# Performance work log

Hardware: AMD Instinct MI355X
Metric: run time of the kernel (lower is better)

The kernel has to match this reference:

```python
import jax, jax.numpy as jnp
import numpy as np

N_HEAD = 16
N_FEAT = 1024
D_HEAD = N_FEAT // N_HEAD


def setup_inputs() -> dict:
    key = jax.random.key(0)
    ks = jax.random.split(key, 12)
    B, L, T = 8, 128, 64
    s = 0.05
    return {
        "q": jax.random.normal(ks[0], (B, 1, N_FEAT), jnp.float32),
        "kv": jax.random.normal(ks[1], (B, L, T, N_FEAT), jnp.float32),
        "Wq": jax.random.normal(ks[2], (D_HEAD, D_HEAD), jnp.float32) * s,
        "bq": jax.random.normal(ks[3], (D_HEAD,), jnp.float32) * s,
        "Wk": jax.random.normal(ks[4], (D_HEAD, D_HEAD), jnp.float32) * s,
        "bk": jax.random.normal(ks[5], (D_HEAD,), jnp.float32) * s,
        "Wv": jax.random.normal(ks[6], (D_HEAD, D_HEAD), jnp.float32) * s,
        "bv": jax.random.normal(ks[7], (D_HEAD,), jnp.float32) * s,
        "Wo": jax.random.normal(ks[8], (N_FEAT, N_FEAT), jnp.float32) * s,
        "bo": jax.random.normal(ks[9], (N_FEAT,), jnp.float32) * s,
    }


def reference(q, kv, Wq, bq, Wk, bk, Wv, bv, Wo, bo):
    B, L, T, D = kv.shape
    H, dh = N_HEAD, D_HEAD
    # mean-pool q over its singleton length dim and kv over T for keys
    qm = q.mean(axis=-2)                      # [B, D]
    km = kv.mean(axis=-2)                     # [B, L, D]
    qh = qm.reshape(B, H, dh)                 # [B, H, dh]
    kh = km.reshape(B, L, H, dh)              # [B, L, H, dh]
    vh = kv.reshape(B, L, T, H, dh)           # [B, L, T, H, dh]
    # per-head linear projections (torch Linear: x @ W.T + b)
    qh = qh @ Wq.T + bq
    kh = kh @ Wk.T + bk
    vh = vh @ Wv.T + bv
    # faithful transpose chain from the original module
    qh = jnp.swapaxes(qh, -2, -3)             # [H, B, dh]  (3D: swaps B and H)
    kh = jnp.swapaxes(kh, -2, -3)             # [B, H, L, dh]
    # broadcasted matmul -> cross-batch attention [B, H, B, L]
    attw = jnp.matmul(qh, jnp.swapaxes(kh, -1, -2)) / jnp.sqrt(jnp.float32(dh))
    attn = jax.nn.softmax(attw, axis=-1)      # [B, H, B, L]
    # value reshuffle: [B,L,T,H,dh] -> [B,H,T,L,dh] -> [B,H,T,dh,L] -> [B,H,T*dh,L]
    v = jnp.swapaxes(vh, -2, -4)
    v = jnp.swapaxes(v, -1, -2)
    v = v.reshape(B, H, T * dh, L)
    ct = jnp.matmul(attn, jnp.swapaxes(v, -1, -2))   # [B, H, B, T*dh]
    ct = ct.reshape(B, H, B, T, dh)
    ct = jnp.swapaxes(ct, -2, -4)                    # [B, T, B, H, dh]
    ct = ct.reshape(B, T, B, H * dh)                 # [B, T, B, D]
    return ct @ Wo.T + bo
```

## Files before the change

### kernel.cpp

```cpp
#include <hip/hip_runtime.h>
#include <hip/hip_bf16.h>

#define BDIM 8
#define LDIM 128
#define TDIM 64
#define NFEAT 1024
#define HNUM 16
#define DH 64

#define GM 4096
#define GN 1024
#define GK 1024

typedef __attribute__((ext_vector_type(8))) short short8;
typedef __attribute__((ext_vector_type(4))) float f32x4;

__device__ __forceinline__ unsigned short f2bf(float x) {
  union { float f; unsigned u; } v; v.f = x;
  unsigned r = v.u + 0x7fffu + ((v.u >> 16) & 1u);
  return (unsigned short)(r >> 16);
}

__device__ __forceinline__ void gload_lds16(const void* g, void* l) {
  __builtin_amdgcn_global_load_lds((const __attribute__((address_space(1))) void*)g,
                                   (__attribute__((address_space(3))) void*)l, 16, 0, 0);
}

__global__ __launch_bounds__(256) void mean_weff_kernel(
    const float* __restrict__ kv, const float* __restrict__ Wo,
    const float* __restrict__ Wv, const float* __restrict__ bv,
    const float* __restrict__ bo, float* __restrict__ km,
    unsigned short* __restrict__ Weff, float* __restrict__ beff) {
  __shared__ float worow[NFEAT];
  __shared__ float red[256];
  const int bl = blockIdx.x;
  const int tid = threadIdx.x;
  {
    const float* src = kv + (size_t)bl * (TDIM * NFEAT) + tid * 4;
    float4 acc = make_float4(0.f, 0.f, 0.f, 0.f);
    for (int t0 = 0; t0 < TDIM; t0 += 8) {
      float4 v[8];
#pragma unroll
      for (int jj = 0; jj < 8; ++jj)
        v[jj] = *(const float4*)(src + (t0 + jj) * NFEAT);
#pragma unroll
      for (int jj = 0; jj < 8; ++jj) {
        acc.x += v[jj].x; acc.y += v[jj].y; acc.z += v[jj].z; acc.w += v[jj].w;
      }
    }
    const float s = 1.f / TDIM;
    const float4 o = make_float4(acc.x * s, acc.y * s, acc.z * s, acc.w * s);
    *(float4*)(km + (size_t)bl * NFEAT + tid * 4) = o;
  }
  {
    const int f = bl;
    *(float4*)(worow + tid * 4) = *(const float4*)(Wo + (size_t)f * NFEAT + tid * 4);
    __syncthreads();
    const int g0 = tid * 4;
    const int hbase = (g0 >> 6) << 6;
    const int i0 = g0 & 63;
    float a0 = 0, a1 = 0, a2 = 0, a3 = 0;
#pragma unroll 4
    for (int d = 0; d < DH; ++d) {
      const float wod = worow[hbase + d];
      const float4 wv4 = *(const float4*)(Wv + d * DH + i0);
      a0 += wod * wv4.x; a1 += wod * wv4.y; a2 += wod * wv4.z; a3 += wod * wv4.w;
    }
    ushort4 pk;
    pk.x = f2bf(a0); pk.y = f2bf(a1); pk.z = f2bf(a2); pk.w = f2bf(a3);
    *(ushort4*)(Weff + (size_t)f * NFEAT + g0) = pk;
    red[tid] = worow[g0 + 0] * bv[i0 + 0] + worow[g0 + 1] * bv[i0 + 1] +
               worow[g0 + 2] * bv[i0 + 2] + worow[g0 + 3] * bv[i0 + 3];
    __syncthreads();
    for (int sft = 128; sft > 0; sft >>= 1) {
      if (tid < sft) red[tid] += red[tid + sft];
      __syncthreads();
    }
    if (tid == 0) beff[f] = bo[f] + red[0];
  }
}

__global__ __launch_bounds__(128) void attn_kernel(const float* __restrict__ q,
                                                   const float* __restrict__ km,
                                                   const float* __restrict__ Wq,
                                                   const float* __restrict__ bq,
                                                   const float* __restrict__ Wk,
                                                   float* __restrict__ attn) {
  __shared__ float qp_s[BDIM * DH];
  __shared__ float qk_s[BDIM * DH];
  __shared__ float sw[BDIM * LDIM];
  __shared__ float mred[BDIM], ired[BDIM];
  const int b1 = blockIdx.x;
  const int h  = blockIdx.y;
  const int tid = threadIdx.x;

  {
    const int e0 = tid * 4;
    const int b2 = e0 >> 6;
    const int d0 = e0 & 63;
    float a0 = bq[d0], a1 = bq[d0 + 1], a2 = bq[d0 + 2], a3 = bq[d0 + 3];
    const float* qrow = q + b2 * NFEAT + h * DH;
#pragma unroll 4
    for (int i = 0; i < DH; ++i) {
      const float qv = qrow[i];
      a0 += qv * Wq[(d0 + 0) * DH + i];
      a1 += qv * Wq[(d0 + 1) * DH + i];
      a2 += qv * Wq[(d0 + 2) * DH + i];
      a3 += qv * Wq[(d0 + 3) * DH + i];
    }
    qp_s[e0 + 0] = a0; qp_s[e0 + 1] = a1; qp_s[e0 + 2] = a2; qp_s[e0 + 3] = a3;
  }
  __syncthreads();
  {
    const int e0 = tid * 4;
    const int b2 = e0 >> 6;
    const int i0 = e0 & 63;
    float a0 = 0, a1 = 0, a2 = 0, a3 = 0;
#pragma unroll 4
    for (int d = 0; d < DH; ++d) {
      const float qpv = qp_s[b2 * DH + d];
      const float4 wk4 = *(const float4*)(Wk + d * DH + i0);
      a0 += qpv * wk4.x; a1 += qpv * wk4.y; a2 += qpv * wk4.z; a3 += qpv * wk4.w;
    }
    qk_s[e0 + 0] = a0; qk_s[e0 + 1] = a1; qk_s[e0 + 2] = a2; qk_s[e0 + 3] = a3;
  }
  __syncthreads();
  {
    const float* kmrow = km + (size_t)(b1 * LDIM + tid) * NFEAT + h * DH;
    float s[8] = {0, 0, 0, 0, 0, 0, 0, 0};
#pragma unroll
    for (int i4 = 0; i4 < DH / 4; ++i4) {
      const float4 kmv = *(const float4*)(kmrow + i4 * 4);
#pragma unroll
      for (int b2 = 0; b2 < 8; ++b2) {
        const float4 qk4 = *(const float4*)(qk_s + b2 * DH + i4 * 4);
        s[b2] += kmv.x * qk4.x + kmv.y * qk4.y + kmv.z * qk4.z + kmv.w * qk4.w;
      }
    }
#pragma unroll
    for (int b2 = 0; b2 < 8; ++b2) sw[b2 * LDIM + tid] = s[b2] * 0.125f;
  }
  __syncthreads();
  {
    const int g = tid >> 4;
    const int r = tid & 15;
    float m = -1e30f;
#pragma unroll
    for (int k = 0; k < 8; ++k) m = fmaxf(m, sw[g * LDIM + r + k * 16]);
#pragma unroll
    for (int s = 1; s < 16; s <<= 1) m = fmaxf(m, __shfl_xor(m, s, 64));
    float ssum = 0.f;
#pragma unroll
    for (int k = 0; k < 8; ++k) ssum += expf(sw[g * LDIM + r + k * 16] - m);
#pragma unroll
    for (int s = 1; s < 16; s <<= 1) ssum += __shfl_xor(ssum, s, 64);
    if (r == 0) { mred[g] = m; ired[g] = 1.f / ssum; }
  }
  __syncthreads();
  {
    float* abase = attn + ((size_t)(b1 * HNUM + h) * BDIM) * LDIM + tid;
#pragma unroll
    for (int b2 = 0; b2 < 8; ++b2)
      abase[b2 * LDIM] = expf(sw[b2 * LDIM + tid] - mred[b2]) * ired[b2];
  }
}

#define HSTRIDE 1032
__global__ __launch_bounds__(64) void pool_kernel(const float* __restrict__ kv,
                                                  const float* __restrict__ attn,
                                                  unsigned short* __restrict__ pooled) {
  __shared__ float wlds[4 * HSTRIDE];
  const int b1 = blockIdx.x;
  const int t = blockIdx.y;
  const int ftile = blockIdx.z;
  const int tid = threadIdx.x;
  {
#pragma unroll
    for (int hg = 0; hg < 4; ++hg) {
      const float* src = attn + ((size_t)(b1 * HNUM + ftile * 4 + hg)) * (BDIM * LDIM);
#pragma unroll
      for (int j = 0; j < 4; ++j) {
        const int idx = (j * 64 + tid) * 4;
        *(float4*)(wlds + hg * HSTRIDE + idx) = *(const float4*)(src + idx);
      }
    }
  }
  __syncthreads();
  const int f = ftile * 256 + tid * 4;
  const int hh = tid >> 4;
  const float* kvbase = kv + ((size_t)b1 * LDIM) * (TDIM * NFEAT) + t * NFEAT + f;
  float4 acc[8];
#pragma unroll
  for (int b2 = 0; b2 < 8; ++b2) acc[b2] = make_float4(0.f, 0.f, 0.f, 0.f);
  const float* wbase = wlds + hh * HSTRIDE;
  for (int l0 = 0; l0 < LDIM; l0 += 8) {
    float4 v[8];
#pragma unroll
    for (int j = 0; j < 8; ++j)
      v[j] = *(const float4*)(kvbase + (size_t)(l0 + j) * (TDIM * NFEAT));
#pragma unroll
    for (int j = 0; j < 8; ++j) {
#pragma unroll
      for (int b2 = 0; b2 < 8; ++b2) {
        const float w = wbase[b2 * LDIM + l0 + j];
        acc[b2].x += w * v[j].x; acc[b2].y += w * v[j].y;
        acc[b2].z += w * v[j].z; acc[b2].w += w * v[j].w;
      }
    }
  }
  unsigned short* obase = pooled + ((size_t)(b1 * TDIM + t) * BDIM) * NFEAT + f;
#pragma unroll
  for (int b2 = 0; b2 < 8; ++b2) {
    ushort4 pk;
    pk.x = f2bf(acc[b2].x); pk.y = f2bf(acc[b2].y);
    pk.z = f2bf(acc[b2].z); pk.w = f2bf(acc[b2].w);
    *(ushort4*)(obase + b2 * NFEAT) = pk;
  }
}

__global__ __launch_bounds__(256) void mfma_gemm(const unsigned short* __restrict__ A,
                                                 const unsigned short* __restrict__ W,
                                                 const float* __restrict__ beff,
                                                 float* __restrict__ out) {
  __shared__ unsigned short As[2][128 * 32];
  __shared__ unsigned short Bs[2][64 * 32];
  const int tid = threadIdx.x;
  const int w = tid >> 6, l = tid & 63;
  const int mBase = blockIdx.y * 128, nBase = blockIdx.x * 64;
  const int wr = w >> 1, wc = w & 1;

  int arow[2], acol[2];
#pragma unroll
  for (int j = 0; j < 2; ++j) {
    const int cid = j * 256 + tid;
    const int r = cid >> 2, c = cid & 3;
    arow[j] = r;
    acol[j] = (c ^ ((r >> 1) & 3)) * 8;
  }
  const int brow = tid >> 2;
  const int bcol = ((tid & 3) ^ ((brow >> 1) & 3)) * 8;

  const int rl = l & 15, ks = l >> 4;
  const int fsel = (ks ^ ((rl >> 1) & 3)) * 16;

  f32x4 acc[4][2] = {};

#pragma unroll
  for (int j = 0; j < 2; ++j)
    gload_lds16(A + (size_t)(mBase + arow[j]) * GK + acol[j],
                (char*)As[0] + (j * 256 + tid) * 16);
  gload_lds16(W + (size_t)(nBase + brow) * GK + bcol, (char*)Bs[0] + tid * 16);
  __syncthreads();

  int cur = 0;
  for (int t = 0; t < GK / 32; ++t) {
    if (t + 1 < GK / 32) {
      const int k0 = (t + 1) * 32;
#pragma unroll
      for (int j = 0; j < 2; ++j)
        gload_lds16(A + (size_t)(mBase + arow[j]) * GK + k0 + acol[j],
                    (char*)As[cur ^ 1] + (j * 256 + tid) * 16);
      gload_lds16(W + (size_t)(nBase + brow) * GK + k0 + bcol,
                  (char*)Bs[cur ^ 1] + tid * 16);
    }
    short8 a[4], b[2];
#pragma unroll
    for (int m = 0; m < 4; ++m)
      a[m] = *(const short8*)((const char*)As[cur] + (wr * 64 + m * 16 + rl) * 64 + fsel);
#pragma unroll
    for (int n = 0; n < 2; ++n)
      b[n] = *(const short8*)((const char*)Bs[cur] + (wc * 32 + n * 16 + rl) * 64 + fsel);
#pragma unroll
    for (int m = 0; m < 4; ++m)
#pragma unroll
      for (int n = 0; n < 2; ++n)
        acc[m][n] = __builtin_amdgcn_mfma_f32_16x16x32_bf16(a[m], b[n], acc[m][n], 0, 0, 0);
    __syncthreads();
    cur ^= 1;
  }

#pragma unroll
  for (int n = 0; n < 2; ++n) {
    const int col = nBase + wc * 32 + n * 16 + rl;
    const float bv = beff[col];
#pragma unroll
    for (int m = 0; m < 4; ++m) {
      const int row0 = mBase + wr * 64 + m * 16 + ks * 4;
#pragma unroll
      for (int j2 = 0; j2 < 4; ++j2)
        out[(size_t)(row0 + j2) * GN + col] = acc[m][n][j2] + bv;
    }
  }
}

extern "C" void kernel_launch(void* const* d_in, const int* in_sizes, int n_in,
                              void* d_out, int out_size, void* d_ws, size_t ws_size,
                              hipStream_t stream) {
  const float* q  = (const float*)d_in[0];
  const float* kv = (const float*)d_in[1];
  const float* Wq = (const float*)d_in[2];
  const float* bq = (const float*)d_in[3];
  const float* Wk = (const float*)d_in[4];
  const float* Wv = (const float*)d_in[6];
  const float* bv = (const float*)d_in[7];
  const float* Wo = (const float*)d_in[8];
  const float* bo = (const float*)d_in[9];
  float* out = (float*)d_out;

  char* ws = (char*)d_ws;
  float*          km     = (float*)ws;
  float*          attnW  = (float*)(ws + (4u << 20));
  float*          beff   = (float*)(ws + (4u << 20) + (512u << 10));
  unsigned short* Weff   = (unsigned short*)(ws + (4u << 20) + (516u << 10));
  unsigned short* pooled = (unsigned short*)(ws + (4u << 20) + (516u << 10) + (2u << 20));

  mean_weff_kernel<<<BDIM * LDIM, 256, 0, stream>>>(kv, Wo, Wv, bv, bo, km, Weff, beff);
  attn_kernel<<<dim3(BDIM, HNUM), 128, 0, stream>>>(q, km, Wq, bq, Wk, attnW);
  pool_kernel<<<dim3(BDIM, TDIM, 4), 64, 0, stream>>>(kv, attnW, pooled);
  mfma_gemm<<<dim3(GN / 64, GM / 128), 256, 0, stream>>>(pooled, Weff, beff, out);
}
```

Before: 137.1 us.

## Fuse attention score computation into mean kernel and softmax into pool kernel

Removes the separate attention kernel. Each mean-pool block now projects its pooled key row through Wk and Wq algebraically and writes raw scores for all heads and query batches. The softmax normalization moves into the pool kernel, which recomputes max and sum per block from the scores. This saves a launch and the km round trip through memory. In exchange, softmax and exp work is repeated across the 64 t-blocks, and the mean kernel does extra per-block matmul work.

```diff
diff --git a/kernel.cpp b/kernel.cpp
--- a/kernel.cpp
+++ b/kernel.cpp
@@ -26,15 +26,23 @@
                                    (__attribute__((address_space(3))) void*)l, 16, 0, 0);
 }
 
-__global__ __launch_bounds__(256) void mean_weff_kernel(
-    const float* __restrict__ kv, const float* __restrict__ Wo,
+__global__ __launch_bounds__(256) void mean_score_weff_kernel(
+    const float* __restrict__ kv, const float* __restrict__ q,
+    const float* __restrict__ Wq, const float* __restrict__ bq,
+    const float* __restrict__ Wk, const float* __restrict__ Wo,
     const float* __restrict__ Wv, const float* __restrict__ bv,
-    const float* __restrict__ bo, float* __restrict__ km,
+    const float* __restrict__ bo, float* __restrict__ scores,
     unsigned short* __restrict__ Weff, float* __restrict__ beff) {
+  __shared__ float km_s[NFEAT];
+  __shared__ float Wk_s[DH * 67];
+  __shared__ float kw_s[HNUM * DH];
+  __shared__ float wqkw_s[HNUM * 66];
+  __shared__ float bqkw_s[HNUM];
   __shared__ float worow[NFEAT];
   __shared__ float red[256];
   const int bl = blockIdx.x;
   const int tid = threadIdx.x;
+
   {
     const float* src = kv + (size_t)bl * (TDIM * NFEAT) + tid * 4;
     float4 acc = make_float4(0.f, 0.f, 0.f, 0.f);
@@ -49,8 +57,53 @@
       }
     }
     const float s = 1.f / TDIM;
-    const float4 o = make_float4(acc.x * s, acc.y * s, acc.z * s, acc.w * s);
-    *(float4*)(km + (size_t)bl * NFEAT + tid * 4) = o;
+    *(float4*)(km_s + tid * 4) = make_float4(acc.x * s, acc.y * s, acc.z * s, acc.w * s);
+  }
+#pragma unroll
+  for (int rep = 0; rep < 4; ++rep) {
+    const int e4 = rep * 256 + tid;
+    const int row = e4 >> 4, c4 = e4 & 15;
+    const float4 v = *(const float4*)(Wk + row * DH + c4 * 4);
+    float* dst = Wk_s + row * 67 + c4 * 4;
+    dst[0] = v.x; dst[1] = v.y; dst[2] = v.z; dst[3] = v.w;
+  }
+  __syncthreads();
+#pragma unroll
+  for (int rep = 0; rep < 4; ++rep) {
+    const int e = rep * 256 + tid;
+    const int h = e >> 6, dd = e & 63;
+    float acc = 0.f;
+#pragma unroll 4
+    for (int d = 0; d < DH; ++d) acc += Wk_s[dd * 67 + d] * km_s[h * 64 + d];
+    kw_s[h * 64 + dd] = acc;
+  }
+  __syncthreads();
+#pragma unroll
+  for (int rep = 0; rep < 4; ++rep) {
+    const int e = rep * 256 + tid;
+    const int h = e >> 6, i = e & 63;
+    float acc = 0.f;
+#pragma unroll 4
+    for (int dd = 0; dd < DH; ++dd) acc += Wq[dd * DH + i] * kw_s[h * 64 + dd];
+    wqkw_s[h * 66 + i] = acc;
+  }
+  if (tid < HNUM) {
+    float acc = 0.f;
+#pragma unroll 4
+    for (int dd = 0; dd < DH; ++dd) acc += bq[dd] * kw_s[tid * 64 + dd];
+    bqkw_s[tid] = acc;
+  }
+  __syncthreads();
+  {
+    const int w = tid >> 6, lane = tid & 63;
+    for (int k = 0; k < 32; ++k) {
+      const int e = w * 32 + k;
+      const int h = e >> 3, b2 = e & 7;
+      float p = q[b2 * NFEAT + h * DH + lane] * wqkw_s[h * 66 + lane];
+#pragma unroll
+      for (int s = 1; s < 64; s <<= 1) p += __shfl_xor(p, s, 64);
+      if (lane == 0) scores[(size_t)bl * 128 + e] = (p + bqkw_s[h]) * 0.125f;
+    }
   }
   {
     const int f = bl;
@@ -80,110 +133,32 @@
   }
 }
 
-__global__ __launch_bounds__(128) void attn_kernel(const float* __restrict__ q,
-                                                   const float* __restrict__ km,
-                                                   const float* __restrict__ Wq,
-                                                   const float* __restrict__ bq,
-                                                   const float* __restrict__ Wk,
-                                                   float* __restrict__ attn) {
-  __shared__ float qp_s[BDIM * DH];
-  __shared__ float qk_s[BDIM * DH];
-  __shared__ float sw[BDIM * LDIM];
-  __shared__ float mred[BDIM], ired[BDIM];
-  const int b1 = blockIdx.x;
-  const int h  = blockIdx.y;
-  const int tid = threadIdx.x;
-
-  {
-    const int e0 = tid * 4;
-    const int b2 = e0 >> 6;
-    const int d0 = e0 & 63;
-    float a0 = bq[d0], a1 = bq[d0 + 1], a2 = bq[d0 + 2], a3 = bq[d0 + 3];
-    const float* qrow = q + b2 * NFEAT + h * DH;
-#pragma unroll 4
-    for (int i = 0; i < DH; ++i) {
-      const float qv = qrow[i];
-      a0 += qv * Wq[(d0 + 0) * DH + i];
-      a1 += qv * Wq[(d0 + 1) * DH + i];
-      a2 += qv * Wq[(d0 + 2) * DH + i];
-      a3 += qv * Wq[(d0 + 3) * DH + i];
-    }
-    qp_s[e0 + 0] = a0; qp_s[e0 + 1] = a1; qp_s[e0 + 2] = a2; qp_s[e0 + 3] = a3;
-  }
-  __syncthreads();
-  {
-    const int e0 = tid * 4;
-    const int b2 = e0 >> 6;
-    const int i0 = e0 & 63;
-    float a0 = 0, a1 = 0, a2 = 0, a3 = 0;
-#pragma unroll 4
-    for (int d = 0; d < DH; ++d) {
-      const float qpv = qp_s[b2 * DH + d];
-      const float4 wk4 = *(const float4*)(Wk + d * DH + i0);
-      a0 += qpv * wk4.x; a1 += qpv * wk4.y; a2 += qpv * wk4.z; a3 += qpv * wk4.w;
-    }
-    qk_s[e0 + 0] = a0; qk_s[e0 + 1] = a1; qk_s[e0 + 2] = a2; qk_s[e0 + 3] = a3;
-  }
-  __syncthreads();
-  {
-    const float* kmrow = km + (size_t)(b1 * LDIM + tid) * NFEAT + h * DH;
-    float s[8] = {0, 0, 0, 0, 0, 0, 0, 0};
-#pragma unroll
-    for (int i4 = 0; i4 < DH / 4; ++i4) {
-      const float4 kmv = *(const float4*)(kmrow + i4 * 4);
-#pragma unroll
-      for (int b2 = 0; b2 < 8; ++b2) {
-        const float4 qk4 = *(const float4*)(qk_s + b2 * DH + i4 * 4);
-        s[b2] += kmv.x * qk4.x + kmv.y * qk4.y + kmv.z * qk4.z + kmv.w * qk4.w;
-      }
-    }
-#pragma unroll
-    for (int b2 = 0; b2 < 8; ++b2) sw[b2 * LDIM + tid] = s[b2] * 0.125f;
-  }
-  __syncthreads();
-  {
-    const int g = tid >> 4;
-    const int r = tid & 15;
-    float m = -1e30f;
-#pragma unroll
-    for (int k = 0; k < 8; ++k) m = fmaxf(m, sw[g * LDIM + r + k * 16]);
-#pragma unroll
-    for (int s = 1; s < 16; s <<= 1) m = fmaxf(m, __shfl_xor(m, s, 64));
-    float ssum = 0.f;
-#pragma unroll
-    for (int k = 0; k < 8; ++k) ssum += expf(sw[g * LDIM + r + k * 16] - m);
-#pragma unroll
-    for (int s = 1; s < 16; s <<= 1) ssum += __shfl_xor(ssum, s, 64);
-    if (r == 0) { mred[g] = m; ired[g] = 1.f / ssum; }
-  }
-  __syncthreads();
-  {
-    float* abase = attn + ((size_t)(b1 * HNUM + h) * BDIM) * LDIM + tid;
-#pragma unroll
-    for (int b2 = 0; b2 < 8; ++b2)
-      abase[b2 * LDIM] = expf(sw[b2 * LDIM + tid] - mred[b2]) * ired[b2];
-  }
-}
-
-#define HSTRIDE 1032
-__global__ __launch_bounds__(64) void pool_kernel(const float* __restrict__ kv,
-                                                  const float* __restrict__ attn,
-                                                  unsigned short* __restrict__ pooled) {
-  __shared__ float wlds[4 * HSTRIDE];
+__global__ __launch_bounds__(64) void pool_kernel(
+    const float* __restrict__ kv, const float* __restrict__ scores,
+    unsigned short* __restrict__ pooled) {
+  __shared__ float wldsT[LDIM * 36];
+  __shared__ float mrow[32], irow[32];
   const int b1 = blockIdx.x;
   const int t = blockIdx.y;
   const int ftile = blockIdx.z;
   const int tid = threadIdx.x;
-  {
-#pragma unroll
-    for (int hg = 0; hg < 4; ++hg) {
-      const float* src = attn + ((size_t)(b1 * HNUM + ftile * 4 + hg)) * (BDIM * LDIM);
-#pragma unroll
-      for (int j = 0; j < 4; ++j) {
-        const int idx = (j * 64 + tid) * 4;
-        *(float4*)(wlds + hg * HSTRIDE + idx) = *(const float4*)(src + idx);
-      }
-    }
+  const float* sc = scores + (size_t)b1 * (LDIM * 128) + ftile * 32;
+  {
+    const int hb = tid & 31, half = tid >> 5;
+    const float* scp = sc + (size_t)(half * 64) * 128 + hb;
+    float m = -1e30f;
+    for (int j = 0; j < 64; ++j) m = fmaxf(m, scp[j * 128]);
+    m = fmaxf(m, __shfl_xor(m, 32, 64));
+    float ssum = 0.f;
+    for (int j = 0; j < 64; ++j) ssum += expf(scp[j * 128] - m);
+    ssum += __shfl_xor(ssum, 32, 64);
+    if (half == 0) { mrow[hb] = m; irow[hb] = 1.f / ssum; }
+  }
+  __syncthreads();
+  for (int rep = 0; rep < 64; ++rep) {
+    const int e = rep * 64 + tid;
+    const int hb = e & 31, l = e >> 5;
+    wldsT[l * 36 + hb] = expf(sc[(size_t)l * 128 + hb] - mrow[hb]) * irow[hb];
   }
   __syncthreads();
   const int f = ftile * 256 + tid * 4;
@@ -192,7 +167,6 @@
   float4 acc[8];
 #pragma unroll
   for (int b2 = 0; b2 < 8; ++b2) acc[b2] = make_float4(0.f, 0.f, 0.f, 0.f);
-  const float* wbase = wlds + hh * HSTRIDE;
   for (int l0 = 0; l0 < LDIM; l0 += 8) {
     float4 v[8];
 #pragma unroll
@@ -200,9 +174,10 @@
       v[j] = *(const float4*)(kvbase + (size_t)(l0 + j) * (TDIM * NFEAT));
 #pragma unroll
     for (int j = 0; j < 8; ++j) {
+      const float* wrow = wldsT + (l0 + j) * 36 + hh * 8;
 #pragma unroll
       for (int b2 = 0; b2 < 8; ++b2) {
-        const float w = wbase[b2 * LDIM + l0 + j];
+        const float w = wrow[b2];
         acc[b2].x += w * v[j].x; acc[b2].y += w * v[j].y;
         acc[b2].z += w * v[j].z; acc[b2].w += w * v[j].w;
       }
@@ -308,14 +283,13 @@
   float* out = (float*)d_out;
 
   char* ws = (char*)d_ws;
-  float*          km     = (float*)ws;
-  float*          attnW  = (float*)(ws + (4u << 20));
-  float*          beff   = (float*)(ws + (4u << 20) + (512u << 10));
-  unsigned short* Weff   = (unsigned short*)(ws + (4u << 20) + (516u << 10));
-  unsigned short* pooled = (unsigned short*)(ws + (4u << 20) + (516u << 10) + (2u << 20));
-
-  mean_weff_kernel<<<BDIM * LDIM, 256, 0, stream>>>(kv, Wo, Wv, bv, bo, km, Weff, beff);
-  attn_kernel<<<dim3(BDIM, HNUM), 128, 0, stream>>>(q, km, Wq, bq, Wk, attnW);
-  pool_kernel<<<dim3(BDIM, TDIM, 4), 64, 0, stream>>>(kv, attnW, pooled);
+  float*          scores = (float*)ws;
+  float*          beff   = (float*)(ws + (1u << 20));
+  unsigned short* Weff   = (unsigned short*)(ws + (1u << 20) + (4u << 10));
+  unsigned short* pooled = (unsigned short*)(ws + (4u << 20));
+
+  mean_score_weff_kernel<<<BDIM * LDIM, 256, 0, stream>>>(
+      kv, q, Wq, bq, Wk, Wo, Wv, bv, bo, scores, Weff, beff);
+  pool_kernel<<<dim3(BDIM, TDIM, 4), 64, 0, stream>>>(kv, scores, pooled);
   mfma_gemm<<<dim3(GN / 64, GM / 128), 256, 0, stream>>>(pooled, Weff, beff, out);
 }
```

New measurement: 156.5 us. 14.2% more time.
